# Kernel tuning notes

Measured on AMD Instinct MI355X. Metric: run time of the kernel, lower is better.

The kernel has to match this reference:

```python
import jax, jax.numpy as jnp
import numpy as np

DIM, H, DH, MLP, ADIM = 512, 8, 64, 2048, 256
B, T = 4, 2048
EPS = 1e-5


def setup_inputs() -> dict:
    key = jax.random.key(0)
    ks = jax.random.split(key, 10)
    s = 0.02
    inner = H * DH
    return {
        "x": jax.random.normal(ks[0], (B, T, DIM), jnp.float32),
        "action_emb": jax.random.normal(ks[1], (B, T, ADIM), jnp.float32),
        "causal_mask": jnp.tril(jnp.ones((T, T), dtype=bool)),
        "Wqkv": jax.random.normal(ks[2], (3 * inner, DIM), jnp.float32) * s,
        "Wout": jax.random.normal(ks[3], (DIM, inner), jnp.float32) * s,
        "bout": jnp.zeros((DIM,), jnp.float32),
        "W1": jax.random.normal(ks[4], (MLP, DIM), jnp.float32) * s,
        "b1": jnp.zeros((MLP,), jnp.float32),
        "W2": jax.random.normal(ks[5], (DIM, MLP), jnp.float32) * s,
        "b2": jnp.zeros((DIM,), jnp.float32),
        # adaLN is zero-init in the module; use small random so modulation is exercised
        "Wmod": jax.random.normal(ks[6], (6 * DIM, ADIM), jnp.float32) * s,
        "bmod": jnp.zeros((6 * DIM,), jnp.float32),
    }


def _layernorm(z):
    mu = jnp.mean(z, axis=-1, keepdims=True)
    var = jnp.var(z, axis=-1, keepdims=True)
    return (z - mu) * jax.lax.rsqrt(var + EPS)


def reference(x, action_emb, causal_mask, Wqkv, Wout, bout, W1, b1, W2, b2, Wmod, bmod):
    b, t, d = x.shape
    mod = jax.nn.silu(action_emb) @ Wmod.T + bmod            # (B,T,6*dim)
    shift1, scale1, gate1, shift2, scale2, gate2 = jnp.split(mod, 6, axis=-1)

    h = _layernorm(x) * (1.0 + scale1) + shift1
    qkv = (h @ Wqkv.T).reshape(b, t, 3, H, DH)
    q, k, v = qkv[:, :, 0], qkv[:, :, 1], qkv[:, :, 2]        # (B,T,H,DH)
    scores = jnp.einsum("bqhd,bkhd->bhqk", q, k) * (DH ** -0.5)
    scores = jnp.where(causal_mask, scores, -jnp.inf)
    attn = jax.nn.softmax(scores, axis=-1)                   # dropout=eval (identity)
    h = jnp.einsum("bhqk,bkhd->bqhd", attn, v).reshape(b, t, H * DH)
    h = h @ Wout.T + bout
    x = x + gate1 * h

    h = _layernorm(x) * (1.0 + scale2) + shift2
    h = jax.nn.gelu(h @ W1.T + b1, approximate=False) @ W2.T + b2
    return x + gate2 * h
```

## Files before the change

kernel.cpp:

```cpp
#include <hip/hip_runtime.h>
#include <math.h>
#include <stdint.h>

#define BB 4
#define TT 2048
#define NTOK 8192
#define DIMD 512
#define HH 8
#define DHH 64
#define MLPD 2048
#define ADIMD 256
#define MODD 3072
#define LNEPS 1e-5f
#define LOG2E_8 0.18033688011112042f
#define PBLK 2176

typedef short short8 __attribute__((ext_vector_type(8)));
typedef unsigned short ushort4v __attribute__((ext_vector_type(4)));
typedef __bf16 bf16x8 __attribute__((ext_vector_type(8)));
typedef float f32x4 __attribute__((ext_vector_type(4)));

static __device__ __forceinline__ unsigned short f2bf(float f) {
    return __builtin_bit_cast(unsigned short, (__bf16)f);
}
static __device__ __forceinline__ float bf2f(unsigned short u) {
    union { unsigned u; float f; } v; v.u = (unsigned)u << 16; return v.f;
}
static __device__ __forceinline__ unsigned pk2bf(float a, float b) {
    return (unsigned)f2bf(a) | ((unsigned)f2bf(b) << 16);
}

static __device__ __forceinline__ f32x4 mfma_bf16(short8 a, short8 b, f32x4 c) {
    return __builtin_amdgcn_mfma_f32_16x16x32_bf16(
        __builtin_bit_cast(bf16x8, a), __builtin_bit_cast(bf16x8, b), c, 0, 0, 0);
}

static __device__ __forceinline__ void gload_lds16(const void* g, void* l) {
    __builtin_amdgcn_global_load_lds(
        (const __attribute__((address_space(1))) unsigned int*)g,
        (__attribute__((address_space(3))) unsigned int*)l, 16, 0, 0);
}

struct CvtArgs {
    const float* s[6];
    unsigned short* d[6];
    int cum[7];
};
__global__ __launch_bounds__(256) void cvt_all(CvtArgs a)
{
    const int i = blockIdx.x * 256 + threadIdx.x;
    if (i >= a.cum[6]) return;
    int seg = 0;
    #pragma unroll
    for (int k = 1; k < 6; k++) seg += (i >= a.cum[k]);
    const int off = i - a.cum[seg];
    float4 v = ((const float4*)a.s[seg])[off];
    if (seg == 5) {
        v.x = v.x / (1.f + __expf(-v.x));
        v.y = v.y / (1.f + __expf(-v.y));
        v.z = v.z / (1.f + __expf(-v.z));
        v.w = v.w / (1.f + __expf(-v.w));
    }
    uint2 o;
    o.x = pk2bf(v.x, v.y);
    o.y = pk2bf(v.z, v.w);
    ((uint2*)a.d[seg])[off] = o;
}

template<int EPI, int BN>
__global__ __launch_bounds__(256, (BN == 128 ? 4 : 6)) void gemm_bf16(
    const unsigned short* __restrict__ A, const unsigned short* __restrict__ Bw,
    const float* __restrict__ bias, const float* __restrict__ res,
    const unsigned short* __restrict__ mod,
    int M, int N, int K,
    void* __restrict__ Cv)
{
    constexpr int MT = (BN == 128) ? 4 : 2;
    constexpr int NPB = BN / 32;
    __shared__ unsigned short As[128 * 64];
    __shared__ unsigned short Bs[BN * 64];

    const int tid = threadIdx.x;
    const int w = tid >> 6, lane = tid & 63;
    const int quad = lane >> 4, l16 = lane & 15;
    const int wrow = (BN == 128) ? (w >> 1) * 64 : w * 32;
    const int wcol = (BN == 128) ? (w & 1) * 64 : 0;

    const int gx = gridDim.x;
    int lin = (int)(blockIdx.y * gx + blockIdx.x);
    const int per = (int)(gx * gridDim.y) >> 3;
    lin = (lin & 7) * per + (lin >> 3);
    const int row0 = (lin / gx) * 128, col0 = (lin % gx) * BN;

    const int srow = tid >> 3;
    const int skc  = (((tid & 7) ^ (srow & 7)) * 8);

    f32x4 acc[MT][4];
    #pragma unroll
    for (int i = 0; i < MT; i++)
        #pragma unroll
        for (int j = 0; j < 4; j++) acc[i][j] = (f32x4){0.f, 0.f, 0.f, 0.f};

    auto stage_async = [&](int k0) {
        #pragma unroll
        for (int p = 0; p < 4; p++)
            gload_lds16(&A[(size_t)(row0 + srow + p * 32) * K + k0 + skc],
                        &As[p * 2048 + tid * 8]);
        #pragma unroll
        for (int p = 0; p < NPB; p++)
            gload_lds16(&Bw[(size_t)(col0 + srow + p * 32) * K + k0 + skc],
                        &Bs[p * 2048 + tid * 8]);
    };

    stage_async(0);
    __syncthreads();

    const int xk = l16 & 7;
    for (int k0 = 0; k0 < K; k0 += 64) {
        #pragma unroll
        for (int ks = 0; ks < 2; ks++) {
            const int cx = ((ks * 4 + quad) ^ xk) * 8;
            short8 af[MT], bf[4];
            #pragma unroll
            for (int mt = 0; mt < MT; mt++)
                af[mt] = *(const short8*)&As[(wrow + mt * 16 + l16) * 64 + cx];
            #pragma unroll
            for (int nt = 0; nt < 4; nt++)
                bf[nt] = *(const short8*)&Bs[(wcol + nt * 16 + l16) * 64 + cx];
            #pragma unroll
            for (int nt = 0; nt < 4; nt++)
                #pragma unroll
                for (int mt = 0; mt < MT; mt++)
                    acc[mt][nt] = mfma_bf16(af[mt], bf[nt], acc[mt][nt]);
        }
        __syncthreads();
        if (k0 + 64 < K) stage_async(k0 + 64);
        __syncthreads();
    }

    float* Cf = (float*)Cv;
    unsigned short* Cb = (unsigned short*)Cv;
    #pragma unroll
    for (int mt = 0; mt < MT; mt++) {
        #pragma unroll
        for (int r = 0; r < 4; r++) {
            const int row = row0 + wrow + mt * 16 + quad * 4 + r;
            #pragma unroll
            for (int nt = 0; nt < 4; nt++) {
                const int col = col0 + wcol + nt * 16 + l16;
                const size_t idx = (size_t)row * N + col;
                const float v = acc[mt][nt][r];
                if (EPI == 0) {
                    Cb[idx] = f2bf(v);
                } else if (EPI == 2) {
                    float t = v + bias[col];
                    Cb[idx] = f2bf(0.5f * t * (1.f + erff(t * 0.70710678118654752f)));
                } else if (EPI == 3) {
                    float t = v + bias[col];
                    Cf[idx] = res[idx] + bf2f(mod[(size_t)row * MODD + 1024 + col]) * t;
                } else if (EPI == 4) {
                    float t = v + bias[col];
                    Cf[idx] = Cf[idx] + bf2f(mod[(size_t)row * MODD + 2560 + col]) * t;
                } else if (EPI == 5) {
                    Cb[idx] = f2bf(v + bias[col]);
                }
            }
        }
    }
}

__global__ __launch_bounds__(256) void adaln_ln(
    const float* __restrict__ src, const unsigned short* __restrict__ mod,
    unsigned short* __restrict__ dst, int shift_off, int scale_off)
{
    const int n = blockIdx.x;
    const int tid = threadIdx.x;
    const float* xr = src + (size_t)n * DIMD;
    float v0 = xr[tid], v1 = xr[tid + 256];
    float s = v0 + v1;
    float q = v0 * v0 + v1 * v1;
    #pragma unroll
    for (int o = 32; o > 0; o >>= 1) {
        s += __shfl_down(s, o);
        q += __shfl_down(q, o);
    }
    __shared__ float sh[8];
    __shared__ float mu_sh, rs_sh;
    const int wid = tid >> 6, lane = tid & 63;
    if (lane == 0) { sh[wid] = s; sh[wid + 4] = q; }
    __syncthreads();
    if (tid == 0) {
        float S = sh[0] + sh[1] + sh[2] + sh[3];
        float Q = sh[4] + sh[5] + sh[6] + sh[7];
        float mu = S * (1.f / DIMD);
        float var = Q * (1.f / DIMD) - mu * mu;
        mu_sh = mu;
        rs_sh = rsqrtf(var + LNEPS);
    }
    __syncthreads();
    const float mu = mu_sh, rs = rs_sh;
    const unsigned short* mrow = mod + (size_t)n * MODD;
    const size_t o0 = (size_t)n * DIMD + tid;
    dst[o0]       = f2bf((v0 - mu) * rs * (1.f + bf2f(mrow[scale_off + tid]))       + bf2f(mrow[shift_off + tid]));
    dst[o0 + 256] = f2bf((v1 - mu) * rs * (1.f + bf2f(mrow[scale_off + tid + 256])) + bf2f(mrow[shift_off + tid + 256]));
}

__global__ __launch_bounds__(256, 5) void attn_mfma(
    const unsigned short* __restrict__ qkv, float* __restrict__ part)
{
    __shared__ unsigned short Kt[64][76];
    __shared__ unsigned short Vt[64][76];
    __shared__ unsigned short Ps[4][16][76];

    const int f = 79 - (int)blockIdx.x;
    int qi, ch;
    if (f < 8)       { qi = f;               ch = 0; }
    else if (f < 24) { const int g = f - 8;  qi = 8 + (g >> 1);  ch = g & 1; }
    else if (f < 48) { const int g = f - 24; qi = 16 + g / 3;    ch = g % 3; }
    else             { const int g = f - 48; qi = 24 + (g >> 2); ch = g & 3; }

    const int h = blockIdx.y, b = blockIdx.z;
    const int tid = threadIdx.x;
    const int w = tid >> 6;
    const int lane = tid & 63;
    const int quad = lane >> 4;
    const int l16 = lane & 15;

    const int qw = qi * 64 + w * 16;
    const size_t tokbase = (size_t)b * TT;

    short8 qf[2];
    {
        const unsigned short* qp = qkv + (tokbase + qw + l16) * 1536 + h * 64 + quad * 8;
        #pragma unroll
        for (int hd = 0; hd < 2; hd++) {
            short8 raw = *(const short8*)(qp + hd * 32);
            short8 fr;
            #pragma unroll
            for (int j = 0; j < 8; j++)
                fr[j] = (short)f2bf(bf2f((unsigned short)raw[j]) * LOG2E_8);
            qf[hd] = fr;
        }
    }

    f32x4 Oa[4];
    float mrun = -INFINITY, lrun = 0.f;
    #pragma unroll
    for (int mt = 0; mt < 4; mt++) Oa[mt] = (f32x4){0.f, 0.f, 0.f, 0.f};

    const int k0t = ch * 8;
    const int k1t = min(k0t + 8, qi + 1);
    const int vk0 = (tid & 31) * 2;
    const int vdb = (tid >> 5) * 8;

    short8 kpre[2], vpre[2];
    auto prefetchKV = [&](int kt) {
        const unsigned short* kb = qkv + (tokbase + (size_t)kt * 64) * 1536 + 512 + h * 64;
        #pragma unroll
        for (int it = 0; it < 2; it++) {
            const int i = tid + it * 256;
            kpre[it] = *(const short8*)(kb + (size_t)(i >> 3) * 1536 + (i & 7) * 8);
        }
        const unsigned short* vb = qkv + (tokbase + (size_t)kt * 64 + vk0) * 1536 + 1024 + h * 64 + vdb;
        vpre[0] = *(const short8*)vb;
        vpre[1] = *(const short8*)(vb + 1536);
    };
    auto storeKV = [&]() {
        #pragma unroll
        for (int it = 0; it < 2; it++) {
            const int i = tid + it * 256;
            *(short8*)&Kt[i >> 3][(i & 7) * 8] = kpre[it];
        }
        #pragma unroll
        for (int j = 0; j < 8; j++) {
            *(unsigned*)&Vt[vdb + j][vk0] =
                (unsigned)(unsigned short)vpre[0][j]
                | ((unsigned)(unsigned short)vpre[1][j] << 16);
        }
    };

    prefetchKV(k0t);
    storeKV();
    __syncthreads();

    for (int kt = k0t; kt < k1t; kt++) {
        const bool haveNext = (kt + 1 < k1t);
        if (haveNext) prefetchKV(kt + 1);

        f32x4 st[4];
        #pragma unroll
        for (int mk = 0; mk < 4; mk++) {
            const short8 a0 = *(const short8*)&Kt[mk * 16 + l16][quad * 8];
            const short8 a1 = *(const short8*)&Kt[mk * 16 + l16][32 + quad * 8];
            st[mk] = (f32x4){0.f, 0.f, 0.f, 0.f};
            st[mk] = mfma_bf16(a0, qf[0], st[mk]);
            st[mk] = mfma_bf16(a1, qf[1], st[mk]);
        }
        if (kt == qi) {
            const int qrel = w * 16 + l16;
            #pragma unroll
            for (int mk = 0; mk < 4; mk++)
                #pragma unroll
                for (int r = 0; r < 4; r++)
                    if (mk * 16 + quad * 4 + r > qrel) st[mk][r] = -INFINITY;
        }
        float tm = -INFINITY;
        #pragma unroll
        for (int mk = 0; mk < 4; mk++)
            #pragma unroll
            for (int r = 0; r < 4; r++) tm = fmaxf(tm, st[mk][r]);
        tm = fmaxf(tm, __shfl_xor(tm, 16));
        tm = fmaxf(tm, __shfl_xor(tm, 32));
        if (!__all(tm <= mrun + 8.0f)) {
            const float mn = fmaxf(mrun, tm);
            const float alpha = __builtin_amdgcn_exp2f(mrun - mn);
            lrun *= alpha;
            #pragma unroll
            for (int mt = 0; mt < 4; mt++) Oa[mt] *= alpha;
            mrun = mn;
        }
        float ts = 0.f;
        #pragma unroll
        for (int mk = 0; mk < 4; mk++) {
            const float p0 = __builtin_amdgcn_exp2f(st[mk][0] - mrun);
            const float p1 = __builtin_amdgcn_exp2f(st[mk][1] - mrun);
            const float p2 = __builtin_amdgcn_exp2f(st[mk][2] - mrun);
            const float p3 = __builtin_amdgcn_exp2f(st[mk][3] - mrun);
            ts += (p0 + p1) + (p2 + p3);
            const unsigned long long pk =
                (unsigned long long)pk2bf(p0, p1)
                | ((unsigned long long)pk2bf(p2, p3) << 32);
            *(unsigned long long*)&Ps[w][l16][mk * 16 + quad * 4] = pk;
        }
        ts += __shfl_xor(ts, 16);
        ts += __shfl_xor(ts, 32);
        lrun += ts;
        __threadfence_block();

        short8 pf[2];
        #pragma unroll
        for (int kc = 0; kc < 2; kc++)
            pf[kc] = *(const short8*)&Ps[w][l16][kc * 32 + quad * 8];
        #pragma unroll
        for (int mt = 0; mt < 4; mt++)
            #pragma unroll
            for (int kc = 0; kc < 2; kc++) {
                const short8 vf = *(const short8*)&Vt[mt * 16 + l16][kc * 32 + quad * 8];
                Oa[mt] = mfma_bf16(vf, pf[kc], Oa[mt]);
            }

        __syncthreads();
        if (haveNext) storeKV();
        __syncthreads();
    }

    float* pO = part + ((size_t)((b * HH + h) * 80 + f)) * PBLK;
    unsigned short* pOb = (unsigned short*)pO;
    #pragma unroll
    for (int mt = 0; mt < 4; mt++) {
        uint2 o;
        o.x = pk2bf(Oa[mt][0], Oa[mt][1]);
        o.y = pk2bf(Oa[mt][2], Oa[mt][3]);
        *(uint2*)&pOb[(w * 16 + l16) * 64 + mt * 16 + quad * 4] = o;
    }
    if (quad == 0) {
        pO[2048 + (w * 16 + l16) * 2]     = mrun;
        pO[2048 + (w * 16 + l16) * 2 + 1] = lrun;
    }
}

__global__ __launch_bounds__(256) void attn_combine(
    const float* __restrict__ part, unsigned short* __restrict__ outb)
{
    const int idx = blockIdx.x * 256 + threadIdx.x;
    const int d4 = idx & 15;
    const int h = (idx >> 4) & 7;
    const int tok = idx >> 7;
    const int t = tok & (TT - 1);
    const int b = tok >> 11;
    const int qi = t >> 6;
    const int nch = (qi >> 3) + 1;
    int cum;
    if (qi < 8)       cum = qi;
    else if (qi < 16) cum = 8 + ((qi - 8) << 1);
    else if (qi < 24) cum = 24 + (qi - 16) * 3;
    else              cum = 48 + ((qi - 24) << 2);
    const int qloc = t & 63;
    const float* base = part + ((size_t)((b * HH + h) * 80 + cum)) * PBLK;

    float M = -INFINITY;
    for (int c = 0; c < nch; c++)
        M = fmaxf(M, base[c * PBLK + 2048 + qloc * 2]);
    float L = 0.f, a0 = 0.f, a1 = 0.f, a2 = 0.f, a3 = 0.f;
    for (int c = 0; c < nch; c++) {
        const float* pc = base + (size_t)c * PBLK;
        const float m = pc[2048 + qloc * 2];
        const float l = pc[2048 + qloc * 2 + 1];
        const float sc = __builtin_amdgcn_exp2f(m - M);
        L += l * sc;
        const uint2 o = *(const uint2*)&((const unsigned short*)pc)[qloc * 64 + d4 * 4];
        a0 += sc * bf2f((unsigned short)(o.x & 0xffffu));
        a1 += sc * bf2f((unsigned short)(o.x >> 16));
        a2 += sc * bf2f((unsigned short)(o.y & 0xffffu));
        a3 += sc * bf2f((unsigned short)(o.y >> 16));
    }
    const float inv = 1.f / L;
    const unsigned long long pk =
        (unsigned long long)pk2bf(a0 * inv, a1 * inv)
        | ((unsigned long long)pk2bf(a2 * inv, a3 * inv) << 32);
    *(unsigned long long*)&outb[(size_t)tok * DIMD + h * 64 + d4 * 4] = pk;
}

extern "C" void kernel_launch(void* const* d_in, const int* in_sizes, int n_in,
                              void* d_out, int out_size, void* d_ws, size_t ws_size,
                              hipStream_t stream)
{
    (void)in_sizes; (void)n_in; (void)out_size; (void)ws_size;

    const float* x    = (const float*)d_in[0];
    const float* aemb = (const float*)d_in[1];
    const float* Wqkv = (const float*)d_in[3];
    const float* Wout = (const float*)d_in[4];
    const float* bout = (const float*)d_in[5];
    const float* W1   = (const float*)d_in[6];
    const float* b1   = (const float*)d_in[7];
    const float* W2   = (const float*)d_in[8];
    const float* b2   = (const float*)d_in[9];
    const float* Wmod = (const float*)d_in[10];
    const float* bmod = (const float*)d_in[11];

    float* out = (float*)d_out;

    char* p = (char*)d_ws;
    unsigned short* modw = (unsigned short*)p; p += (size_t)NTOK * MODD * 2;
    unsigned short* h12  = (unsigned short*)p; p += (size_t)NTOK * DIMD * 2;
    unsigned short* qkvb = (unsigned short*)p; p += (size_t)NTOK * 1536 * 2;
    unsigned short* attw = (unsigned short*)p; p += (size_t)NTOK * DIMD * 2;
    unsigned short* hid  = qkvb;
    unsigned short* sact = (unsigned short*)p; p += (size_t)NTOK * ADIMD * 2;
    unsigned short* wq = (unsigned short*)p;   p += (size_t)1536 * 512 * 2;
    unsigned short* wo = (unsigned short*)p;   p += (size_t)512 * 512 * 2;
    unsigned short* w1 = (unsigned short*)p;   p += (size_t)2048 * 512 * 2;
    unsigned short* w2 = (unsigned short*)p;   p += (size_t)512 * 2048 * 2;
    unsigned short* wm = (unsigned short*)p;   p += (size_t)3072 * 256 * 2;
    p = (char*)(((uintptr_t)p + 255) & ~(uintptr_t)255);
    float* part = (float*)p;

    CvtArgs ca;
    ca.s[0] = Wqkv; ca.d[0] = wq;
    ca.s[1] = Wout; ca.d[1] = wo;
    ca.s[2] = W1;   ca.d[2] = w1;
    ca.s[3] = W2;   ca.d[3] = w2;
    ca.s[4] = Wmod; ca.d[4] = wm;
    ca.s[5] = aemb; ca.d[5] = sact;
    const int n4s[6] = {1536 * 512 / 4, 512 * 512 / 4, 2048 * 512 / 4,
                        512 * 2048 / 4, 3072 * 256 / 4, NTOK * ADIMD / 4};
    ca.cum[0] = 0;
    for (int i = 0; i < 6; i++) ca.cum[i + 1] = ca.cum[i] + n4s[i];
    cvt_all<<<(ca.cum[6] + 255) / 256, 256, 0, stream>>>(ca);

    gemm_bf16<5, 128><<<dim3(MODD / 128, NTOK / 128), 256, 0, stream>>>(
        sact, wm, bmod, nullptr, nullptr, NTOK, MODD, ADIMD, modw);

    adaln_ln<<<NTOK, 256, 0, stream>>>(x, modw, h12, 0, 512);

    gemm_bf16<0, 128><<<dim3(1536 / 128, NTOK / 128), 256, 0, stream>>>(
        h12, wq, nullptr, nullptr, nullptr, NTOK, 1536, DIMD, qkvb);

    attn_mfma<<<dim3(80, HH, BB), 256, 0, stream>>>(qkvb, part);
    attn_combine<<<NTOK * HH * 16 / 256, 256, 0, stream>>>(part, attw);

    gemm_bf16<3, 64><<<dim3(DIMD / 64, NTOK / 128), 256, 0, stream>>>(
        attw, wo, bout, x, modw, NTOK, DIMD, DIMD, out);

    adaln_ln<<<NTOK, 256, 0, stream>>>(out, modw, h12, 1536, 2048);

    gemm_bf16<2, 128><<<dim3(MLPD / 128, NTOK / 128), 256, 0, stream>>>(
        h12, w1, b1, nullptr, nullptr, NTOK, MLPD, DIMD, hid);

    gemm_bf16<4, 64><<<dim3(DIMD / 64, NTOK / 128), 256, 0, stream>>>(
        hid, w2, b2, nullptr, modw, NTOK, DIMD, MLPD, out);
}
```

Measured before the change: 294.7 us.

## Store mid-block residual in bf16 and raise wave priority around attention MFMAs

The residual stream after the attention block is now written as bf16 into a new workspace buffer instead of fp32 into the output. The second adaLN and the final MLP epilogue read that bf16 buffer, and the final GEMM writes out directly instead of doing a read-modify-write on out. This halves the traffic for the intermediate residual but adds bf16 rounding error to the residual that feeds the output. Separately, s_setprio is raised around the QK and PV MFMA loops in the attention kernel to favour matrix issue across waves.

```diff
diff --git a/kernel.cpp b/kernel.cpp
--- a/kernel.cpp
+++ b/kernel.cpp
@@ -157,10 +157,11 @@
                     Cb[idx] = f2bf(0.5f * t * (1.f + erff(t * 0.70710678118654752f)));
                 } else if (EPI == 3) {
                     float t = v + bias[col];
-                    Cf[idx] = res[idx] + bf2f(mod[(size_t)row * MODD + 1024 + col]) * t;
+                    Cb[idx] = f2bf(res[idx] + bf2f(mod[(size_t)row * MODD + 1024 + col]) * t);
                 } else if (EPI == 4) {
                     float t = v + bias[col];
-                    Cf[idx] = Cf[idx] + bf2f(mod[(size_t)row * MODD + 2560 + col]) * t;
+                    const unsigned short* xm = (const unsigned short*)res;
+                    Cf[idx] = bf2f(xm[idx]) + bf2f(mod[(size_t)row * MODD + 2560 + col]) * t;
                 } else if (EPI == 5) {
                     Cb[idx] = f2bf(v + bias[col]);
                 }
@@ -169,14 +170,21 @@
     }
 }
 
+template<int BF16IN>
 __global__ __launch_bounds__(256) void adaln_ln(
-    const float* __restrict__ src, const unsigned short* __restrict__ mod,
+    const void* __restrict__ src, const unsigned short* __restrict__ mod,
     unsigned short* __restrict__ dst, int shift_off, int scale_off)
 {
     const int n = blockIdx.x;
     const int tid = threadIdx.x;
-    const float* xr = src + (size_t)n * DIMD;
-    float v0 = xr[tid], v1 = xr[tid + 256];
+    float v0, v1;
+    if (BF16IN) {
+        const unsigned short* xr = (const unsigned short*)src + (size_t)n * DIMD;
+        v0 = bf2f(xr[tid]); v1 = bf2f(xr[tid + 256]);
+    } else {
+        const float* xr = (const float*)src + (size_t)n * DIMD;
+        v0 = xr[tid]; v1 = xr[tid + 256];
+    }
     float s = v0 + v1;
     float q = v0 * v0 + v1 * v1;
     #pragma unroll
@@ -288,6 +296,7 @@
         if (haveNext) prefetchKV(kt + 1);
 
         f32x4 st[4];
+        __builtin_amdgcn_s_setprio(1);
         #pragma unroll
         for (int mk = 0; mk < 4; mk++) {
             const short8 a0 = *(const short8*)&Kt[mk * 16 + l16][quad * 8];
@@ -296,6 +305,7 @@
             st[mk] = mfma_bf16(a0, qf[0], st[mk]);
             st[mk] = mfma_bf16(a1, qf[1], st[mk]);
         }
+        __builtin_amdgcn_s_setprio(0);
         if (kt == qi) {
             const int qrel = w * 16 + l16;
             #pragma unroll
@@ -341,6 +351,7 @@
         #pragma unroll
         for (int kc = 0; kc < 2; kc++)
             pf[kc] = *(const short8*)&Ps[w][l16][kc * 32 + quad * 8];
+        __builtin_amdgcn_s_setprio(1);
         #pragma unroll
         for (int mt = 0; mt < 4; mt++)
             #pragma unroll
@@ -348,6 +359,7 @@
                 const short8 vf = *(const short8*)&Vt[mt * 16 + l16][kc * 32 + quad * 8];
                 Oa[mt] = mfma_bf16(vf, pf[kc], Oa[mt]);
             }
+        __builtin_amdgcn_s_setprio(0);
 
         __syncthreads();
         if (haveNext) storeKV();
@@ -437,6 +449,7 @@
     unsigned short* qkvb = (unsigned short*)p; p += (size_t)NTOK * 1536 * 2;
     unsigned short* attw = (unsigned short*)p; p += (size_t)NTOK * DIMD * 2;
     unsigned short* hid  = qkvb;
+    unsigned short* xmid = (unsigned short*)p; p += (size_t)NTOK * DIMD * 2;
     unsigned short* sact = (unsigned short*)p; p += (size_t)NTOK * ADIMD * 2;
     unsigned short* wq = (unsigned short*)p;   p += (size_t)1536 * 512 * 2;
     unsigned short* wo = (unsigned short*)p;   p += (size_t)512 * 512 * 2;
@@ -462,7 +475,7 @@
     gemm_bf16<5, 128><<<dim3(MODD / 128, NTOK / 128), 256, 0, stream>>>(
         sact, wm, bmod, nullptr, nullptr, NTOK, MODD, ADIMD, modw);
 
-    adaln_ln<<<NTOK, 256, 0, stream>>>(x, modw, h12, 0, 512);
+    adaln_ln<0><<<NTOK, 256, 0, stream>>>(x, modw, h12, 0, 512);
 
     gemm_bf16<0, 128><<<dim3(1536 / 128, NTOK / 128), 256, 0, stream>>>(
         h12, wq, nullptr, nullptr, nullptr, NTOK, 1536, DIMD, qkvb);
@@ -471,13 +484,13 @@
     attn_combine<<<NTOK * HH * 16 / 256, 256, 0, stream>>>(part, attw);
 
     gemm_bf16<3, 64><<<dim3(DIMD / 64, NTOK / 128), 256, 0, stream>>>(
-        attw, wo, bout, x, modw, NTOK, DIMD, DIMD, out);
-
-    adaln_ln<<<NTOK, 256, 0, stream>>>(out, modw, h12, 1536, 2048);
+        attw, wo, bout, x, modw, NTOK, DIMD, DIMD, xmid);
+
+    adaln_ln<1><<<NTOK, 256, 0, stream>>>(xmid, modw, h12, 1536, 2048);
 
     gemm_bf16<2, 128><<<dim3(MLPD / 128, NTOK / 128), 256, 0, stream>>>(
         h12, w1, b1, nullptr, nullptr, NTOK, MLPD, DIMD, hid);
 
     gemm_bf16<4, 64><<<dim3(DIMD / 64, NTOK / 128), 256, 0, stream>>>(
-        hid, w2, b2, nullptr, modw, NTOK, DIMD, MLPD, out);
-}
+        hid, w2, b2, (const float*)xmid, modw, NTOK, DIMD, MLPD, out);
+}
```

Result: no change. 296.3 us (+0.6%).
